# Kernel tuning notes

Measured on AMD Instinct MI355X. Metric: run time of the kernel, lower is better.

The kernel has to match this reference:

```python
import jax, jax.numpy as jnp
import numpy as np

N, E, G = 50000, 600000, 64
MUL = 16        # hidden multiplicity: 16x0e + 16x1o -> node feature dim 16 + 48 = 64
MIN_ = 8        # input multiplicity: 8x0e + 8x1o -> input dim 8 + 24 = 32
NUM_LAYERS = 3
INV_S3 = float(1.0 / np.sqrt(3.0))   # CG norm for 1o x 1o -> 0e (dot)
INV_S2 = float(1.0 / np.sqrt(2.0))   # CG norm for 1o x 1o -> 1o (cross)
NORM_S = float(1.0 / np.sqrt(2 * MUL * MUL))  # fan-in: two paths feed 0e output
NORM_V = float(1.0 / np.sqrt(3 * MUL * MUL))  # fan-in: three paths feed 1o output
INV_LIN_IN = float(1.0 / np.sqrt(MIN_))
INV_LIN_OUT = float(1.0 / np.sqrt(MUL))


def _pair(a, b, W):
    # a: [E,u], b: [E,v], W: [u,v,w] -> [E,w]; opt_einsum keeps intermediates at E*MUL^2
    return jnp.einsum('eu,ev,uvw->ew', a, b, W)


def _tp(s1, v1, s2, v2, W):
    """FullyConnectedTensorProduct for (16x0e+16x1o) x (16x0e+16x1o) -> (16x0e+16x1o).
    s*: [E,MUL] scalars, v*: [E,MUL,3] vectors, W: [5,MUL,MUL,MUL] per-path weights."""
    # 0e outputs: 0e*0e->0e  and  1o.1o->0e (dot product, CG = delta/sqrt(3))
    p1 = _pair(s1, s2, W[0])
    p4 = sum(_pair(v1[:, :, i], v2[:, :, i], W[3]) for i in range(3))
    out_s = (p1 + p4 * INV_S3) * NORM_S
    # 1o outputs: 0e*1o->1o, 1o*0e->1o, 1o x 1o -> 1o (cross, CG = eps/sqrt(2))
    p2 = jnp.einsum('eu,evi,uvw->ewi', s1, v2, W[1])
    p3 = jnp.einsum('eui,ev,uvw->ewi', v1, s2, W[2])
    cyc = [(1, 2), (2, 0), (0, 1)]  # eps_ijk: out_k = a_i b_j - a_j b_i
    p5 = jnp.stack([_pair(v1[:, :, i], v2[:, :, j], W[4]) - _pair(v1[:, :, j], v2[:, :, i], W[4])
                    for (i, j) in cyc], axis=-1)
    out_v = (p2 + p3 + p5 * INV_S2) * NORM_V
    return out_s, out_v


def _gate(s, v):
    # irreps-aware Gate: scalars through SiLU, vectors gated by sigmoid of matching scalars
    return jax.nn.silu(s), v * jax.nn.sigmoid(s)[:, :, None]


def setup_inputs() -> dict:
    key = jax.random.key(0)
    ks = jax.random.split(key, 8)
    x = jax.random.normal(ks[0], (N, MIN_ + 3 * MIN_), dtype=jnp.float32)
    row = jax.random.randint(ks[1], (E,), 0, N, dtype=jnp.int32)
    col = jax.random.randint(ks[2], (E,), 0, N, dtype=jnp.int32)
    batch_idx = jnp.sort(jax.random.randint(ks[3], (N,), 0, G, dtype=jnp.int32))
    w_in0 = jax.random.normal(ks[4], (MIN_, MUL), dtype=jnp.float32)   # input Linear 0e->0e
    w_in1 = jax.random.normal(ks[5], (MIN_, MUL), dtype=jnp.float32)   # input Linear 1o->1o
    tp_w = jax.random.normal(ks[6], (NUM_LAYERS, 5, MUL, MUL, MUL), dtype=jnp.float32)
    w_out0 = jax.random.normal(ks[7], (MUL, 1), dtype=jnp.float32)     # readout Linear 0e->0e
    return dict(x=x, row=row, col=col, batch_idx=batch_idx,
                w_in0=w_in0, w_in1=w_in1, tp_w=tp_w, w_out0=w_out0)


def reference(x, row, col, batch_idx, w_in0, w_in1, tp_w, w_out0):
    n = x.shape[0]
    # irreps Linear input projection (per-irrep multiplicity mixing, e3nn-normalized)
    s = (x[:, :MIN_] @ w_in0) * INV_LIN_IN                                  # [N,MUL]
    v = jnp.einsum('nui,uw->nwi', x[:, MIN_:].reshape(n, MIN_, 3), w_in1) * INV_LIN_IN  # [N,MUL,3]
    for l in range(NUM_LAYERS):
        ms, mv = _tp(s[row], v[row], s[col], v[col], tp_w[l])  # gather + CG tensor product
        s = jax.ops.segment_sum(ms, row, num_segments=n)       # scatter-add to destination
        v = jax.ops.segment_sum(mv, row, num_segments=n)
        s, v = _gate(s, v)
    node_out = (s @ w_out0)[:, 0] * INV_LIN_OUT                # readout Linear -> 1x0e
    energy = jax.ops.segment_sum(node_out, batch_idx, num_segments=G)  # per-graph energy
    return energy
```

## Files before the change

kernel.cpp:

```cpp
#include <hip/hip_runtime.h>

#define N_NODES 50000
#define N_EDGES 600000
#define N_GRAPHS 64
#define N_TILES (N_EDGES / 16)
#define EDGE_GRID 2048

#define SCAN_T 1024
#define SCAN_C 49

#define INV_LIN_IN  0.35355339059327373f
#define INV_LIN_OUT 0.25f
#define C_INV_S3    0.5773502691896258f
#define C_INV_S2    0.7071067811865476f
#define C_NORM_S    0.04419417382415922f
#define C_NORM_V    0.036084391824351615f

#define ALPHA      0.03125f
#define W_UNSCALE  1024.0f

typedef __attribute__((ext_vector_type(8))) _Float16 h16x8;
typedef __attribute__((ext_vector_type(4))) _Float16 h16x4;
typedef __attribute__((ext_vector_type(2))) _Float16 h16x2;
typedef __attribute__((ext_vector_type(4))) float f32x4;

__global__ void hist_kernel(const int* __restrict__ row, int* __restrict__ counts) {
    int e = blockIdx.x * 256 + threadIdx.x;
    if (e < N_EDGES) atomicAdd(&counts[row[e]], 1);
}

__global__ __launch_bounds__(SCAN_T)
void scan_one_kernel(const int* __restrict__ counts, int* __restrict__ cursor) {
    __shared__ int sm[SCAN_T];
    int t = threadIdx.x;
    int base = t * SCAN_C;
    int local[SCAN_C];
    int sum = 0;
#pragma unroll
    for (int k = 0; k < SCAN_C; ++k) {
        int i = base + k;
        int v = (i < N_NODES) ? counts[i] : 0;
        local[k] = sum;
        sum += v;
    }
    sm[t] = sum;
    __syncthreads();
    for (int s = 1; s < SCAN_T; s <<= 1) {
        int add = (t >= s) ? sm[t - s] : 0;
        __syncthreads();
        sm[t] += add;
        __syncthreads();
    }
    int tbase = (t > 0) ? sm[t - 1] : 0;
#pragma unroll
    for (int k = 0; k < SCAN_C; ++k) {
        int i = base + k;
        if (i < N_NODES) cursor[i] = tbase + local[k];
    }
}

__global__ void scatter_kernel(const int* __restrict__ row, const int* __restrict__ col,
                               int* __restrict__ cursor, int* __restrict__ sortedRC) {
    int e = blockIdx.x * 256 + threadIdx.x;
    if (e < N_EDGES) {
        int n = row[e];
        int pos = atomicAdd(&cursor[n], 1);
        sortedRC[pos] = n | (col[e] << 16);
    }
}

__global__ void init_kernel(const float* __restrict__ x,
                            const float* __restrict__ w_in0,
                            const float* __restrict__ w_in1,
                            const float* __restrict__ tp_w,
                            h16x4* __restrict__ featH,
                            _Float16* __restrict__ wh,
                            int* __restrict__ counts,
                            float* __restrict__ energy,
                            float4* __restrict__ acc) {
    int gid = blockIdx.x * 256 + threadIdx.x;

    if (gid < 64) energy[gid] = 0.f;
    if (gid < N_NODES) counts[gid] = 0;

    for (int idx = gid; idx < N_NODES * 16; idx += 61440)
        acc[idx] = make_float4(0.f, 0.f, 0.f, 0.f);

    if (gid < 3 * 20480) {
        int i = gid;
        int j    = i & 7;
        int t1   = i >> 3;
        int lane = t1 & 63;
        int t2   = t1 >> 6;
        int c    = t2 & 7;
        int t3   = t2 >> 3;
        int slot = t3 % 5;
        int l    = t3 / 5;
        int p = (slot == 0) ? 1 : (slot == 1) ? 2 : (slot == 2) ? 4 : (slot == 3) ? 0 : 3;
        int kk = c * 32 + (lane >> 4) * 8 + j;
        int u = kk >> 4, v = kk & 15, n = lane & 15;
        float scale;
        if      (p == 0) scale = C_NORM_S;
        else if (p == 3) scale = C_INV_S3 * C_NORM_S;
        else if (p == 4) scale = C_INV_S2 * C_NORM_V;
        else             scale = C_NORM_V;
        if (l > 0) scale *= W_UNSCALE;
        float val = tp_w[(size_t)(l * 5 + p) * 4096 + u * 256 + v * 16 + n] * scale;
        wh[i] = (_Float16)val;
    }

    if (gid < N_NODES) {
        const float* xp = x + (size_t)gid * 32;
        float xs[8], xvx[8], xvy[8], xvz[8];
#pragma unroll
        for (int u = 0; u < 8; ++u) xs[u] = xp[u];
#pragma unroll
        for (int u = 0; u < 8; ++u) {
            xvx[u] = xp[8 + 3 * u + 0];
            xvy[u] = xp[8 + 3 * u + 1];
            xvz[u] = xp[8 + 3 * u + 2];
        }
#pragma unroll
        for (int w = 0; w < 16; ++w) {
            float s = 0.f, vx = 0.f, vy = 0.f, vz = 0.f;
#pragma unroll
            for (int u = 0; u < 8; ++u) {
                float a0 = w_in0[u * 16 + w];
                float a1 = w_in1[u * 16 + w];
                s  += xs[u]  * a0;
                vx += xvx[u] * a1;
                vy += xvy[u] * a1;
                vz += xvz[u] * a1;
            }
            h16x4 o;
            o.x = (_Float16)(s  * INV_LIN_IN);
            o.y = (_Float16)(vx * INV_LIN_IN);
            o.z = (_Float16)(vy * INV_LIN_IN);
            o.w = (_Float16)(vz * INV_LIN_IN);
            featH[(size_t)gid * 16 + w] = o;
        }
    }
}

__global__ __launch_bounds__(256, 4)
void edge_tp_kernel(const h16x4* __restrict__ feat,
                    float* __restrict__ out,
                    const int* __restrict__ sortedRC,
                    const _Float16* __restrict__ wh) {
    __shared__ h16x8 sW[1024];

    const int t = threadIdx.x;
    {
        const int4* src = (const int4*)wh;
        int4* dst = (int4*)sW;
#pragma unroll
        for (int i = 0; i < 4; ++i) dst[t + 256 * i] = src[t + 256 * i];
    }
    __syncthreads();

    const int lane = t & 63;
    const int wave = t >> 6;
    const int q = lane >> 4;
    const int m = lane & 15;
    const int v0 = (q & 1) * 8;

    const h16x8* gw = ((const h16x8*)wh) + 1024;

    const int gw_id = blockIdx.x * 4 + wave;
    const int nw = gridDim.x * 4;
    int tile = (int)(((long long)gw_id * N_TILES) / nw);
    const int tileEnd = (int)(((long long)(gw_id + 1) * N_TILES) / nw);
    if (tile >= tileEnd) return;

    int rc = sortedRC[tile * 16 + m];
    h16x4 Bt[8];
    {
        const h16x4* bp = feat + (size_t)(((unsigned)rc) >> 16) * 16 + v0;
#pragma unroll
        for (int k = 0; k < 8; ++k) Bt[k] = bp[k];
    }

    for (; tile < tileEnd; ++tile) {
        const int myR = rc & 0xFFFF;
        const int nt = tile + 1;
        const int nrc = (nt < tileEnd) ? sortedRC[nt * 16 + m] : rc;

        h16x2 Bs[4], Bx[4], By[4], Bz[4];
#pragma unroll
        for (int k = 0; k < 4; ++k) {
            Bs[k].x = Bt[2 * k].x; Bs[k].y = Bt[2 * k + 1].x;
            Bx[k].x = Bt[2 * k].y; Bx[k].y = Bt[2 * k + 1].y;
            By[k].x = Bt[2 * k].z; By[k].y = Bt[2 * k + 1].z;
            Bz[k].x = Bt[2 * k].w; Bz[k].y = Bt[2 * k + 1].w;
        }

        f32x4 acc_s = {0.f, 0.f, 0.f, 0.f};
        f32x4 acc_x = {0.f, 0.f, 0.f, 0.f};
        f32x4 acc_y = {0.f, 0.f, 0.f, 0.f};
        f32x4 acc_z = {0.f, 0.f, 0.f, 0.f};

        const h16x4* ap = feat + (size_t)myR * 16;

#pragma unroll 4
        for (int c = 0; c < 8; ++c) {
            h16x8 w4f = gw[(0 * 8 + c) * 64 + lane];
            h16x8 w0f = gw[(1 * 8 + c) * 64 + lane];
            h16x8 w3f = gw[(2 * 8 + c) * 64 + lane];
            h16x8 w1f = sW[(0 * 8 + c) * 64 + lane];
            h16x8 w2f = sW[(1 * 8 + c) * 64 + lane];

            h16x4 A = ap[2 * c + (q >> 1)];
            h16x2 s2; s2.x = A.x; s2.y = A.x;
            h16x2 x2; x2.x = A.y; x2.y = A.y;
            h16x2 y2; y2.x = A.z; y2.y = A.z;
            h16x2 z2; z2.x = A.w; z2.y = A.w;

            union { h16x8 v; h16x2 h[4]; } z;

#pragma unroll
            for (int k = 0; k < 4; ++k) z.h[k] = s2 * Bs[k];
            acc_s = __builtin_amdgcn_mfma_f32_16x16x32_f16(z.v, w0f, acc_s, 0, 0, 0);

#pragma unroll
            for (int k = 0; k < 4; ++k)
                z.h[k] = x2 * Bx[k] + y2 * By[k] + z2 * Bz[k];
            acc_s = __builtin_amdgcn_mfma_f32_16x16x32_f16(z.v, w3f, acc_s, 0, 0, 0);

#pragma unroll
            for (int k = 0; k < 4; ++k) z.h[k] = s2 * Bx[k];
            acc_x = __builtin_amdgcn_mfma_f32_16x16x32_f16(z.v, w1f, acc_x, 0, 0, 0);
#pragma unroll
            for (int k = 0; k < 4; ++k) z.h[k] = x2 * Bs[k];
            acc_x = __builtin_amdgcn_mfma_f32_16x16x32_f16(z.v, w2f, acc_x, 0, 0, 0);
#pragma unroll
            for (int k = 0; k < 4; ++k) z.h[k] = y2 * Bz[k] - z2 * By[k];
            acc_x = __builtin_amdgcn_mfma_f32_16x16x32_f16(z.v, w4f, acc_x, 0, 0, 0);

#pragma unroll
            for (int k = 0; k < 4; ++k) z.h[k] = s2 * By[k];
            acc_y = __builtin_amdgcn_mfma_f32_16x16x32_f16(z.v, w1f, acc_y, 0, 0, 0);
#pragma unroll
            for (int k = 0; k < 4; ++k) z.h[k] = y2 * Bs[k];
            acc_y = __builtin_amdgcn_mfma_f32_16x16x32_f16(z.v, w2f, acc_y, 0, 0, 0);
#pragma unroll
            for (int k = 0; k < 4; ++k) z.h[k] = z2 * Bx[k] - x2 * Bz[k];
            acc_y = __builtin_amdgcn_mfma_f32_16x16x32_f16(z.v, w4f, acc_y, 0, 0, 0);

#pragma unroll
            for (int k = 0; k < 4; ++k) z.h[k] = s2 * Bz[k];
            acc_z = __builtin_amdgcn_mfma_f32_16x16x32_f16(z.v, w1f, acc_z, 0, 0, 0);
#pragma unroll
            for (int k = 0; k < 4; ++k) z.h[k] = z2 * Bs[k];
            acc_z = __builtin_amdgcn_mfma_f32_16x16x32_f16(z.v, w2f, acc_z, 0, 0, 0);
#pragma unroll
            for (int k = 0; k < 4; ++k) z.h[k] = x2 * By[k] - y2 * Bx[k];
            acc_z = __builtin_amdgcn_mfma_f32_16x16x32_f16(z.v, w4f, acc_z, 0, 0, 0);
        }

        {
            const h16x4* nbp = feat + (size_t)(((unsigned)nrc) >> 16) * 16 + v0;
#pragma unroll
            for (int k = 0; k < 8; ++k) Bt[k] = nbp[k];
        }

        int prevR = __shfl(myR, (lane + 63) & 63);
        int flag = (m == 0) || (myR != prevR);
        unsigned long long bal = __ballot(flag != 0);
        unsigned mask16 = (unsigned)(bal & 0xFFFFull);

        int nseg = __popc(mask16);
        unsigned rem = mask16;
        for (int s = 0; s < nseg; ++s) {
            int lo = __ffs(rem) - 1;
            rem &= rem - 1;
            int hi = rem ? (__ffs(rem) - 1) : 16;
            float ps = 0.f, px = 0.f, py = 0.f, pz = 0.f;
#pragma unroll
            for (int r = 0; r < 4; ++r) {
                int ei = q * 4 + r;
                bool in = (ei >= lo) && (ei < hi);
                ps += in ? acc_s[r] : 0.f;
                px += in ? acc_x[r] : 0.f;
                py += in ? acc_y[r] : 0.f;
                pz += in ? acc_z[r] : 0.f;
            }
            ps += __shfl_xor(ps, 16); ps += __shfl_xor(ps, 32);
            px += __shfl_xor(px, 16); px += __shfl_xor(px, 32);
            py += __shfl_xor(py, 16); py += __shfl_xor(py, 32);
            pz += __shfl_xor(pz, 16); pz += __shfl_xor(pz, 32);
            int node = __shfl(myR, lo);
            float val = (q == 0) ? ps : (q == 1) ? px : (q == 2) ? py : pz;
            atomicAdd(out + (size_t)node * 64 + m * 4 + q, val);
        }

        rc = nrc;
    }
}

__global__ void gate_half_kernel(float4* __restrict__ acc,
                                 h16x4* __restrict__ featH) {
    int i = blockIdx.x * 256 + threadIdx.x;
    if (i >= N_NODES * 16) return;
    float4 f = acc[i];
    float g = ALPHA / (1.f + __expf(-f.x));
    h16x4 o;
    o.x = (_Float16)(f.x * g);
    o.y = (_Float16)(f.y * g);
    o.z = (_Float16)(f.z * g);
    o.w = (_Float16)(f.w * g);
    featH[i] = o;
    acc[i] = make_float4(0.f, 0.f, 0.f, 0.f);
}

__global__ void gate_readout_kernel(const float4* __restrict__ feat,
                                    const int* __restrict__ batch_idx,
                                    const float* __restrict__ w_out,
                                    float* __restrict__ energy) {
    __shared__ float bins[N_GRAPHS];
    int t = threadIdx.x;
    if (t < N_GRAPHS) bins[t] = 0.f;
    __syncthreads();
    int n = blockIdx.x * 256 + t;
    if (n < N_NODES) {
        const float4* f = feat + (size_t)n * 16;
        float acc = 0.f;
#pragma unroll
        for (int w = 0; w < 16; ++w) {
            float s = f[w].x;
            float silu = s / (1.f + __expf(-s));
            acc += silu * w_out[w];
        }
        atomicAdd(&bins[batch_idx[n]], acc * INV_LIN_OUT);
    }
    __syncthreads();
    if (t < N_GRAPHS) atomicAdd(&energy[t], bins[t]);
}

extern "C" void kernel_launch(void* const* d_in, const int* in_sizes, int n_in,
                              void* d_out, int out_size, void* d_ws, size_t ws_size,
                              hipStream_t stream) {
    const float* x         = (const float*)d_in[0];
    const int*   row       = (const int*)d_in[1];
    const int*   col       = (const int*)d_in[2];
    const int*   batch_idx = (const int*)d_in[3];
    const float* w_in0     = (const float*)d_in[4];
    const float* w_in1     = (const float*)d_in[5];
    const float* tp_w      = (const float*)d_in[6];
    const float* w_out0    = (const float*)d_in[7];
    float* energy = (float*)d_out;

    float*    acc   = (float*)d_ws;
    _Float16* featA = (_Float16*)(acc + (size_t)N_NODES * 64);
    _Float16* featB = featA + (size_t)N_NODES * 64;
    _Float16* wh    = featB + (size_t)N_NODES * 64;
    int* sortedRC = (int*)(wh + 3 * 20480);
    int* counts  = (int*)featB;
    int* cursor  = counts + N_NODES;

    init_kernel<<<(3 * 20480 + 255) / 256, 256, 0, stream>>>(
        x, w_in0, w_in1, tp_w, (h16x4*)featA, wh, counts, energy, (float4*)acc);

    hist_kernel<<<(N_EDGES + 255) / 256, 256, 0, stream>>>(row, counts);
    scan_one_kernel<<<1, SCAN_T, 0, stream>>>(counts, cursor);
    scatter_kernel<<<(N_EDGES + 255) / 256, 256, 0, stream>>>(row, col, cursor, sortedRC);

    _Float16* fin = featA;
    _Float16* fnext = featB;
    for (int l = 0; l < 3; ++l) {
        edge_tp_kernel<<<EDGE_GRID, 256, 0, stream>>>(
            (const h16x4*)fin, acc, sortedRC, wh + (size_t)l * 20480);
        if (l < 2) {
            gate_half_kernel<<<(N_NODES * 16 + 255) / 256, 256, 0, stream>>>(
                (float4*)acc, (h16x4*)fnext);
            _Float16* tmp = fin; fin = fnext; fnext = tmp;
        } else {
            gate_readout_kernel<<<(N_NODES + 255) / 256, 256, 0, stream>>>(
                (const float4*)acc, batch_idx, w_out0, energy);
        }
    }
}
```

Baseline: 488.1 us.

## Process two edge tiles per iteration to share weight loads across tiles

The edge tensor-product loop now handles two 16-edge tiles per iteration. Each set of per-chunk weight fragments loaded from global and LDS feeds both tiles' MFMAs, halving weight traffic per tile and exposing two independent MFMA chains. The software prefetch of the next tile's gather is removed, and the chunk loop is no longer unrolled (unroll 1). This roughly doubles accumulator and B-operand register use, which under launch_bounds(256,4) may cause spills or cut occupancy.

```diff
diff --git a/kernel.cpp b/kernel.cpp
--- a/kernel.cpp
+++ b/kernel.cpp
@@ -142,6 +142,111 @@
     }
 }
 
+static __device__ __forceinline__ void tp_chunk(
+    h16x4 A,
+    const h16x2 Bs[4], const h16x2 Bx[4], const h16x2 By[4], const h16x2 Bz[4],
+    h16x8 w0f, h16x8 w1f, h16x8 w2f, h16x8 w3f, h16x8 w4f,
+    f32x4& acc_s, f32x4& acc_x, f32x4& acc_y, f32x4& acc_z)
+{
+    h16x2 s2; s2.x = A.x; s2.y = A.x;
+    h16x2 x2; x2.x = A.y; x2.y = A.y;
+    h16x2 y2; y2.x = A.z; y2.y = A.z;
+    h16x2 z2; z2.x = A.w; z2.y = A.w;
+
+    union { h16x8 v; h16x2 h[4]; } z;
+
+#pragma unroll
+    for (int k = 0; k < 4; ++k) z.h[k] = s2 * Bs[k];
+    acc_s = __builtin_amdgcn_mfma_f32_16x16x32_f16(z.v, w0f, acc_s, 0, 0, 0);
+
+#pragma unroll
+    for (int k = 0; k < 4; ++k) z.h[k] = x2 * Bx[k] + y2 * By[k] + z2 * Bz[k];
+    acc_s = __builtin_amdgcn_mfma_f32_16x16x32_f16(z.v, w3f, acc_s, 0, 0, 0);
+
+#pragma unroll
+    for (int k = 0; k < 4; ++k) z.h[k] = s2 * Bx[k];
+    acc_x = __builtin_amdgcn_mfma_f32_16x16x32_f16(z.v, w1f, acc_x, 0, 0, 0);
+#pragma unroll
+    for (int k = 0; k < 4; ++k) z.h[k] = x2 * Bs[k];
+    acc_x = __builtin_amdgcn_mfma_f32_16x16x32_f16(z.v, w2f, acc_x, 0, 0, 0);
+#pragma unroll
+    for (int k = 0; k < 4; ++k) z.h[k] = y2 * Bz[k] - z2 * By[k];
+    acc_x = __builtin_amdgcn_mfma_f32_16x16x32_f16(z.v, w4f, acc_x, 0, 0, 0);
+
+#pragma unroll
+    for (int k = 0; k < 4; ++k) z.h[k] = s2 * By[k];
+    acc_y = __builtin_amdgcn_mfma_f32_16x16x32_f16(z.v, w1f, acc_y, 0, 0, 0);
+#pragma unroll
+    for (int k = 0; k < 4; ++k) z.h[k] = y2 * Bs[k];
+    acc_y = __builtin_amdgcn_mfma_f32_16x16x32_f16(z.v, w2f, acc_y, 0, 0, 0);
+#pragma unroll
+    for (int k = 0; k < 4; ++k) z.h[k] = z2 * Bx[k] - x2 * Bz[k];
+    acc_y = __builtin_amdgcn_mfma_f32_16x16x32_f16(z.v, w4f, acc_y, 0, 0, 0);
+
+#pragma unroll
+    for (int k = 0; k < 4; ++k) z.h[k] = s2 * Bz[k];
+    acc_z = __builtin_amdgcn_mfma_f32_16x16x32_f16(z.v, w1f, acc_z, 0, 0, 0);
+#pragma unroll
+    for (int k = 0; k < 4; ++k) z.h[k] = z2 * Bs[k];
+    acc_z = __builtin_amdgcn_mfma_f32_16x16x32_f16(z.v, w2f, acc_z, 0, 0, 0);
+#pragma unroll
+    for (int k = 0; k < 4; ++k) z.h[k] = x2 * By[k] - y2 * Bx[k];
+    acc_z = __builtin_amdgcn_mfma_f32_16x16x32_f16(z.v, w4f, acc_z, 0, 0, 0);
+}
+
+static __device__ __forceinline__ void gather_B(
+    const h16x4* __restrict__ feat, int rc, int v0,
+    h16x2 Bs[4], h16x2 Bx[4], h16x2 By[4], h16x2 Bz[4])
+{
+    h16x4 Bt[8];
+    const h16x4* bp = feat + (size_t)(((unsigned)rc) >> 16) * 16 + v0;
+#pragma unroll
+    for (int k = 0; k < 8; ++k) Bt[k] = bp[k];
+#pragma unroll
+    for (int k = 0; k < 4; ++k) {
+        Bs[k].x = Bt[2 * k].x; Bs[k].y = Bt[2 * k + 1].x;
+        Bx[k].x = Bt[2 * k].y; Bx[k].y = Bt[2 * k + 1].y;
+        By[k].x = Bt[2 * k].z; By[k].y = Bt[2 * k + 1].z;
+        Bz[k].x = Bt[2 * k].w; Bz[k].y = Bt[2 * k + 1].w;
+    }
+}
+
+static __device__ __forceinline__ void seg_epilogue(
+    int myR, int lane, int q, int m,
+    const f32x4& acc_s, const f32x4& acc_x, const f32x4& acc_y, const f32x4& acc_z,
+    float* __restrict__ out)
+{
+    int prevR = __shfl(myR, (lane + 63) & 63);
+    int flag = (m == 0) || (myR != prevR);
+    unsigned long long bal = __ballot(flag != 0);
+    unsigned mask16 = (unsigned)(bal & 0xFFFFull);
+
+    int nseg = __popc(mask16);
+    unsigned rem = mask16;
+    for (int s = 0; s < nseg; ++s) {
+        int lo = __ffs(rem) - 1;
+        rem &= rem - 1;
+        int hi = rem ? (__ffs(rem) - 1) : 16;
+        float ps = 0.f, px = 0.f, py = 0.f, pz = 0.f;
+#pragma unroll
+        for (int r = 0; r < 4; ++r) {
+            int ei = q * 4 + r;
+            bool in = (ei >= lo) && (ei < hi);
+            ps += in ? acc_s[r] : 0.f;
+            px += in ? acc_x[r] : 0.f;
+            py += in ? acc_y[r] : 0.f;
+            pz += in ? acc_z[r] : 0.f;
+        }
+        ps += __shfl_xor(ps, 16); ps += __shfl_xor(ps, 32);
+        px += __shfl_xor(px, 16); px += __shfl_xor(px, 32);
+        py += __shfl_xor(py, 16); py += __shfl_xor(py, 32);
+        pz += __shfl_xor(pz, 16); pz += __shfl_xor(pz, 32);
+        int node = __shfl(myR, lo);
+        float val = (q == 0) ? ps : (q == 1) ? px : (q == 2) ? py : pz;
+        atomicAdd(out + (size_t)node * 64 + m * 4 + q, val);
+    }
+}
+
 __global__ __launch_bounds__(256, 4)
 void edge_tp_kernel(const h16x4* __restrict__ feat,
                     float* __restrict__ out,
@@ -170,38 +275,27 @@
     const int nw = gridDim.x * 4;
     int tile = (int)(((long long)gw_id * N_TILES) / nw);
     const int tileEnd = (int)(((long long)(gw_id + 1) * N_TILES) / nw);
-    if (tile >= tileEnd) return;
-
-    int rc = sortedRC[tile * 16 + m];
-    h16x4 Bt[8];
-    {
-        const h16x4* bp = feat + (size_t)(((unsigned)rc) >> 16) * 16 + v0;
-#pragma unroll
-        for (int k = 0; k < 8; ++k) Bt[k] = bp[k];
-    }
-
-    for (; tile < tileEnd; ++tile) {
-        const int myR = rc & 0xFFFF;
-        const int nt = tile + 1;
-        const int nrc = (nt < tileEnd) ? sortedRC[nt * 16 + m] : rc;
-
-        h16x2 Bs[4], Bx[4], By[4], Bz[4];
-#pragma unroll
-        for (int k = 0; k < 4; ++k) {
-            Bs[k].x = Bt[2 * k].x; Bs[k].y = Bt[2 * k + 1].x;
-            Bx[k].x = Bt[2 * k].y; Bx[k].y = Bt[2 * k + 1].y;
-            By[k].x = Bt[2 * k].z; By[k].y = Bt[2 * k + 1].z;
-            Bz[k].x = Bt[2 * k].w; Bz[k].y = Bt[2 * k + 1].w;
-        }
-
-        f32x4 acc_s = {0.f, 0.f, 0.f, 0.f};
-        f32x4 acc_x = {0.f, 0.f, 0.f, 0.f};
-        f32x4 acc_y = {0.f, 0.f, 0.f, 0.f};
-        f32x4 acc_z = {0.f, 0.f, 0.f, 0.f};
-
-        const h16x4* ap = feat + (size_t)myR * 16;
-
-#pragma unroll 4
+
+    for (; tile + 1 < tileEnd; tile += 2) {
+        const int rc0 = sortedRC[tile * 16 + m];
+        const int rc1 = sortedRC[(tile + 1) * 16 + m];
+        const int myR0 = rc0 & 0xFFFF;
+        const int myR1 = rc1 & 0xFFFF;
+
+        h16x2 Bs0[4], Bx0[4], By0[4], Bz0[4];
+        h16x2 Bs1[4], Bx1[4], By1[4], Bz1[4];
+        gather_B(feat, rc0, v0, Bs0, Bx0, By0, Bz0);
+        gather_B(feat, rc1, v0, Bs1, Bx1, By1, Bz1);
+
+        f32x4 as0 = {0.f,0.f,0.f,0.f}, ax0 = {0.f,0.f,0.f,0.f};
+        f32x4 ay0 = {0.f,0.f,0.f,0.f}, az0 = {0.f,0.f,0.f,0.f};
+        f32x4 as1 = {0.f,0.f,0.f,0.f}, ax1 = {0.f,0.f,0.f,0.f};
+        f32x4 ay1 = {0.f,0.f,0.f,0.f}, az1 = {0.f,0.f,0.f,0.f};
+
+        const h16x4* ap0 = feat + (size_t)myR0 * 16;
+        const h16x4* ap1 = feat + (size_t)myR1 * 16;
+
+#pragma unroll 1
         for (int c = 0; c < 8; ++c) {
             h16x8 w4f = gw[(0 * 8 + c) * 64 + lane];
             h16x8 w0f = gw[(1 * 8 + c) * 64 + lane];
@@ -209,91 +303,41 @@
             h16x8 w1f = sW[(0 * 8 + c) * 64 + lane];
             h16x8 w2f = sW[(1 * 8 + c) * 64 + lane];
 
-            h16x4 A = ap[2 * c + (q >> 1)];
-            h16x2 s2; s2.x = A.x; s2.y = A.x;
-            h16x2 x2; x2.x = A.y; x2.y = A.y;
-            h16x2 y2; y2.x = A.z; y2.y = A.z;
-            h16x2 z2; z2.x = A.w; z2.y = A.w;
-
-            union { h16x8 v; h16x2 h[4]; } z;
-
-#pragma unroll
-            for (int k = 0; k < 4; ++k) z.h[k] = s2 * Bs[k];
-            acc_s = __builtin_amdgcn_mfma_f32_16x16x32_f16(z.v, w0f, acc_s, 0, 0, 0);
-
-#pragma unroll
-            for (int k = 0; k < 4; ++k)
-                z.h[k] = x2 * Bx[k] + y2 * By[k] + z2 * Bz[k];
-            acc_s = __builtin_amdgcn_mfma_f32_16x16x32_f16(z.v, w3f, acc_s, 0, 0, 0);
-
-#pragma unroll
-            for (int k = 0; k < 4; ++k) z.h[k] = s2 * Bx[k];
-            acc_x = __builtin_amdgcn_mfma_f32_16x16x32_f16(z.v, w1f, acc_x, 0, 0, 0);
-#pragma unroll
-            for (int k = 0; k < 4; ++k) z.h[k] = x2 * Bs[k];
-            acc_x = __builtin_amdgcn_mfma_f32_16x16x32_f16(z.v, w2f, acc_x, 0, 0, 0);
-#pragma unroll
-            for (int k = 0; k < 4; ++k) z.h[k] = y2 * Bz[k] - z2 * By[k];
-            acc_x = __builtin_amdgcn_mfma_f32_16x16x32_f16(z.v, w4f, acc_x, 0, 0, 0);
-
-#pragma unroll
-            for (int k = 0; k < 4; ++k) z.h[k] = s2 * By[k];
-            acc_y = __builtin_amdgcn_mfma_f32_16x16x32_f16(z.v, w1f, acc_y, 0, 0, 0);
-#pragma unroll
-            for (int k = 0; k < 4; ++k) z.h[k] = y2 * Bs[k];
-            acc_y = __builtin_amdgcn_mfma_f32_16x16x32_f16(z.v, w2f, acc_y, 0, 0, 0);
-#pragma unroll
-            for (int k = 0; k < 4; ++k) z.h[k] = z2 * Bx[k] - x2 * Bz[k];
-            acc_y = __builtin_amdgcn_mfma_f32_16x16x32_f16(z.v, w4f, acc_y, 0, 0, 0);
-
-#pragma unroll
-            for (int k = 0; k < 4; ++k) z.h[k] = s2 * Bz[k];
-            acc_z = __builtin_amdgcn_mfma_f32_16x16x32_f16(z.v, w1f, acc_z, 0, 0, 0);
-#pragma unroll
-            for (int k = 0; k < 4; ++k) z.h[k] = z2 * Bs[k];
-            acc_z = __builtin_amdgcn_mfma_f32_16x16x32_f16(z.v, w2f, acc_z, 0, 0, 0);
-#pragma unroll
-            for (int k = 0; k < 4; ++k) z.h[k] = x2 * By[k] - y2 * Bx[k];
-            acc_z = __builtin_amdgcn_mfma_f32_16x16x32_f16(z.v, w4f, acc_z, 0, 0, 0);
-        }
-
-        {
-            const h16x4* nbp = feat + (size_t)(((unsigned)nrc) >> 16) * 16 + v0;
-#pragma unroll
-            for (int k = 0; k < 8; ++k) Bt[k] = nbp[k];
-        }
-
-        int prevR = __shfl(myR, (lane + 63) & 63);
-        int flag = (m == 0) || (myR != prevR);
-        unsigned long long bal = __ballot(flag != 0);
-        unsigned mask16 = (unsigned)(bal & 0xFFFFull);
-
-        int nseg = __popc(mask16);
-        unsigned rem = mask16;
-        for (int s = 0; s < nseg; ++s) {
-            int lo = __ffs(rem) - 1;
-            rem &= rem - 1;
-            int hi = rem ? (__ffs(rem) - 1) : 16;
-            float ps = 0.f, px = 0.f, py = 0.f, pz = 0.f;
-#pragma unroll
-            for (int r = 0; r < 4; ++r) {
-                int ei = q * 4 + r;
-                bool in = (ei >= lo) && (ei < hi);
-                ps += in ? acc_s[r] : 0.f;
-                px += in ? acc_x[r] : 0.f;
-                py += in ? acc_y[r] : 0.f;
-                pz += in ? acc_z[r] : 0.f;
-            }
-            ps += __shfl_xor(ps, 16); ps += __shfl_xor(ps, 32);
-            px += __shfl_xor(px, 16); px += __shfl_xor(px, 32);
-            py += __shfl_xor(py, 16); py += __shfl_xor(py, 32);
-            pz += __shfl_xor(pz, 16); pz += __shfl_xor(pz, 32);
-            int node = __shfl(myR, lo);
-            float val = (q == 0) ? ps : (q == 1) ? px : (q == 2) ? py : pz;
-            atomicAdd(out + (size_t)node * 64 + m * 4 + q, val);
-        }
-
-        rc = nrc;
+            h16x4 A0 = ap0[2 * c + (q >> 1)];
+            h16x4 A1 = ap1[2 * c + (q >> 1)];
+
+            tp_chunk(A0, Bs0, Bx0, By0, Bz0, w0f, w1f, w2f, w3f, w4f, as0, ax0, ay0, az0);
+            tp_chunk(A1, Bs1, Bx1, By1, Bz1, w0f, w1f, w2f, w3f, w4f, as1, ax1, ay1, az1);
+        }
+
+        seg_epilogue(myR0, lane, q, m, as0, ax0, ay0, az0, out);
+        seg_epilogue(myR1, lane, q, m, as1, ax1, ay1, az1, out);
+    }
+
+    if (tile < tileEnd) {
+        const int rc0 = sortedRC[tile * 16 + m];
+        const int myR0 = rc0 & 0xFFFF;
+
+        h16x2 Bs0[4], Bx0[4], By0[4], Bz0[4];
+        gather_B(feat, rc0, v0, Bs0, Bx0, By0, Bz0);
+
+        f32x4 as0 = {0.f,0.f,0.f,0.f}, ax0 = {0.f,0.f,0.f,0.f};
+        f32x4 ay0 = {0.f,0.f,0.f,0.f}, az0 = {0.f,0.f,0.f,0.f};
+
+        const h16x4* ap0 = feat + (size_t)myR0 * 16;
+
+#pragma unroll 1
+        for (int c = 0; c < 8; ++c) {
+            h16x8 w4f = gw[(0 * 8 + c) * 64 + lane];
+            h16x8 w0f = gw[(1 * 8 + c) * 64 + lane];
+            h16x8 w3f = gw[(2 * 8 + c) * 64 + lane];
+            h16x8 w1f = sW[(0 * 8 + c) * 64 + lane];
+            h16x8 w2f = sW[(1 * 8 + c) * 64 + lane];
+            h16x4 A0 = ap0[2 * c + (q >> 1)];
+            tp_chunk(A0, Bs0, Bx0, By0, Bz0, w0f, w1f, w2f, w3f, w4f, as0, ax0, ay0, az0);
+        }
+
+        seg_epilogue(myR0, lane, q, m, as0, ax0, ay0, az0, out);
     }
 }
 
```

Result: faster. 478.0 us (-2.1%).
